# Kernel tuning notes

Measured on AMD Instinct MI355X. Metric: run time of the kernel, lower is better.

## Reference

```python
import jax, jax.numpy as jnp
import numpy as np

NHEAD, HEAD_DIM, UNFOLD = 16, 64, 3
SCALE = np.float32(1.0 / np.sqrt(HEAD_DIM))


def setup_inputs() -> dict:
    key = jax.random.key(0)
    ks = jax.random.split(key, 10)
    B, C, N, L, aL = 1, 256, 64, 256, 2
    D = NHEAD * HEAD_DIM  # 1024
    return {
        "x": jax.random.normal(ks[0], (B, C, N, L, 1), dtype=jnp.float32),
        "ax": jax.random.normal(ks[1], (B, C, N, aL, L), dtype=jnp.float32),
        "wq": jax.random.normal(ks[2], (D, C), dtype=jnp.float32) * 0.02,
        "bq": jax.random.normal(ks[3], (D,), dtype=jnp.float32) * 0.02,
        "wk": jax.random.normal(ks[4], (D, C), dtype=jnp.float32) * 0.02,
        "bk": jax.random.normal(ks[5], (D,), dtype=jnp.float32) * 0.02,
        "wv": jax.random.normal(ks[6], (D, C), dtype=jnp.float32) * 0.02,
        "bv": jax.random.normal(ks[7], (D,), dtype=jnp.float32) * 0.02,
        "wo": jax.random.normal(ks[8], (C, D), dtype=jnp.float32) * 0.02,
        "bo": jax.random.normal(ks[9], (C,), dtype=jnp.float32) * 0.02,
    }


def _proj(x, w, b):
    # x: [B,C,N,L], w: [D,C] -> [B,D,N,L]  (1x1x1 Conv3d == pointwise GEMM)
    return jnp.einsum('bcnl,dc->bdnl', x, w) + b[None, :, None, None]


def reference(x, ax, wq, bq, wk, bk, wv, bv, wo, bo):
    B, C, N, L, _ = x.shape
    x4 = x[..., 0]  # [B,C,N,L]
    q = _proj(x4, wq, bq).reshape(B, NHEAD, HEAD_DIM, N, 1, L)
    k4 = _proj(x4, wk, bk)
    v4 = _proj(x4, wv, bv)

    def unfold(t):
        # F.unfold kernel (3,1), padding (1,0) along N, then the original's
        # .view(B, nhead, head_dim, N, 3, L) applied to [B, C*3, N*L]
        tp = jnp.pad(t, ((0, 0), (0, 0), (1, 1), (0, 0)))
        tw = jnp.stack([tp[:, :, i:i + N, :] for i in range(UNFOLD)], axis=2)  # [B,D,3,N,L]
        return tw.reshape(B, NHEAD, HEAD_DIM, UNFOLD, N, L).reshape(
            B, NHEAD, HEAD_DIM, N, UNFOLD, L)

    k = unfold(k4)
    v = unfold(v4)

    aL = ax.shape[3]
    ak = (jnp.einsum('bcnal,dc->bdnal', ax, wk)
          + bk[None, :, None, None, None]).reshape(B, NHEAD, HEAD_DIM, N, aL, L)
    av = (jnp.einsum('bcnal,dc->bdnal', ax, wv)
          + bv[None, :, None, None, None]).reshape(B, NHEAD, HEAD_DIM, N, aL, L)
    k = jnp.concatenate([k, ak], axis=4)  # [B,H,d,N,3+aL,L]
    v = jnp.concatenate([v, av], axis=4)

    scores = (q * k).sum(2, keepdims=True) * SCALE        # [B,H,1,N,W,L]
    alphas = jax.nn.softmax(scores, axis=4)               # dropout=eval -> identity
    att = (alphas * v).sum(4).reshape(B, NHEAD * HEAD_DIM, N, L)
    out = jnp.einsum('bdnl,cd->bcnl', att, wo) + bo[None, :, None, None]
    return out[..., None]  # [B,nhid,N,L,1]
```

## Files before the change

kernel.cpp:

```cpp
#include <hip/hip_runtime.h>
#include <hip/hip_bf16.h>
#include <stdint.h>

#define N_HEAD 16
#define HDIM 64
#define C_IN 256
#define D_MODEL 1024
#define N_SP 64
#define L_SP 256
#define A_L 2
#define MS (N_SP * L_SP)
#define MA (N_SP * A_L * L_SP)
#define MT (MS + MA)
#define ATT_SCALE 0.125f
#define AUXP 136
#define CTP 136

typedef __attribute__((ext_vector_type(8))) short bf16x8;
typedef __attribute__((ext_vector_type(4))) float f32x4;
typedef __attribute__((ext_vector_type(8))) unsigned short u16x8;
typedef __attribute__((ext_vector_type(4))) unsigned int u32x4;

static __device__ __forceinline__ __hip_bfloat16 f2bf(float v) { return __float2bfloat16(v); }
static __device__ __forceinline__ unsigned short bfbits(float v) {
    union { __hip_bfloat16 h; unsigned short u; } cv;
    cv.h = __float2bfloat16(v);
    return cv.u;
}
static __device__ __forceinline__ float s2f(short u) {
    union { unsigned int i; float f; } c;
    c.i = ((unsigned int)(unsigned short)u) << 16;
    return c.f;
}

__global__ __launch_bounds__(256) void prep_weights(
    const float* __restrict__ wq, const float* __restrict__ bq,
    const float* __restrict__ wk, const float* __restrict__ bk,
    const float* __restrict__ wv, const float* __restrict__ bv,
    const float* __restrict__ wo,
    __hip_bfloat16* __restrict__ Wqkv, float* __restrict__ BiasQKV,
    __hip_bfloat16* __restrict__ WoB)
{
    int idx = blockIdx.x * 256 + threadIdx.x;
    int row = idx >> 8, col = idx & 255;
    const float* w = (row < D_MODEL) ? wq : (row < 2 * D_MODEL) ? wk : wv;
    Wqkv[idx] = f2bf(w[(size_t)(row & (D_MODEL - 1)) * C_IN + col]);
    if (col == 0) {
        const float* b = (row < D_MODEL) ? bq : (row < 2 * D_MODEL) ? bk : bv;
        BiasQKV[row] = b[row & (D_MODEL - 1)];
    }
    if (idx < C_IN * D_MODEL) WoB[idx] = f2bf(wo[idx]);
}

__global__ __launch_bounds__(256) void transpose_in(
    const float* __restrict__ x, const float* __restrict__ ax,
    __hip_bfloat16* __restrict__ XtAll)
{
    __shared__ float tile[32][33];
    const int tx = threadIdx.x, ty = threadIdx.y;
    const int bx = blockIdx.x;
    const float* src; int M, m0, drow0;
    if (bx < MS / 32) { src = x;  M = MS; m0 = bx * 32;              drow0 = m0; }
    else              { src = ax; M = MA; m0 = (bx - MS / 32) * 32;  drow0 = MS + m0; }
    const int c0 = blockIdx.y * 32;
#pragma unroll
    for (int j = 0; j < 32; j += 8)
        tile[ty + j][tx] = src[(size_t)(c0 + ty + j) * M + m0 + tx];
    __syncthreads();
#pragma unroll
    for (int j = 0; j < 32; j += 8)
        XtAll[(size_t)(drow0 + ty + j) * C_IN + c0 + tx] = f2bf(tile[tx][ty + j]);
}

__global__ __launch_bounds__(256) void gemm_proj(
    const __hip_bfloat16* __restrict__ A,
    const __hip_bfloat16* __restrict__ B,
    __hip_bfloat16* __restrict__ C,
    const float* __restrict__ bias,
    int M, int N, int K)
{
    __shared__ __align__(16) char lds[128 * CTP * 2];
    __hip_bfloat16* As = (__hip_bfloat16*)lds;
    __hip_bfloat16* Bs = As + 128 * 64;
    __hip_bfloat16* Ct = (__hip_bfloat16*)lds;

    const int tid = threadIdx.x;
    const int lane = tid & 63;
    const int w = tid >> 6;
    const int wr = w >> 1, wc = w & 1;
    const int fr = lane & 15, fq = lane >> 4;

    const int nwg = gridDim.x * gridDim.y;
    const int lin = blockIdx.y * gridDim.x + blockIdx.x;
    const int qq = nwg >> 3, rr = nwg & 7;
    const int xcd = lin & 7, ix = lin >> 3;
    const int nlin = (xcd < rr) ? xcd * (qq + 1) + ix
                                : rr * (qq + 1) + (xcd - rr) * qq + ix;
    const int bx = nlin % gridDim.x, by = nlin / gridDim.x;

    const int i0 = by * 128, j0 = bx * 128;
    const int srow = tid >> 3, sch = (tid & 7) << 3;
    const int scolsw = sch ^ ((srow & 7) << 3);
    const int rdsw = (fr & 7) << 3;

    f32x4 acc[4][4];
#pragma unroll
    for (int a = 0; a < 4; ++a)
#pragma unroll
        for (int b = 0; b < 4; ++b) acc[a][b] = (f32x4){0.f, 0.f, 0.f, 0.f};

    for (int k0 = 0; k0 < K; k0 += 64) {
        u32x4 ra[4], rb[4];
#pragma unroll
        for (int is = 0; is < 4; ++is) {
            int row = is * 32 + srow;
            ra[is] = *(const u32x4*)(A + (size_t)(i0 + row) * K + k0 + sch);
            rb[is] = *(const u32x4*)(B + (size_t)(j0 + row) * K + k0 + sch);
        }
#pragma unroll
        for (int is = 0; is < 4; ++is) {
            int row = is * 32 + srow;
            *(u32x4*)(As + row * 64 + scolsw) = ra[is];
            *(u32x4*)(Bs + row * 64 + scolsw) = rb[is];
        }
        __syncthreads();
#pragma unroll
        for (int kk = 0; kk < 64; kk += 32) {
            bf16x8 af[4], bb[4];
#pragma unroll
            for (int mi = 0; mi < 4; ++mi)
                af[mi] = *(const bf16x8*)(As + (wr * 64 + mi * 16 + fr) * 64 + ((kk + fq * 8) ^ rdsw));
#pragma unroll
            for (int ni = 0; ni < 4; ++ni)
                bb[ni] = *(const bf16x8*)(Bs + (wc * 64 + ni * 16 + fr) * 64 + ((kk + fq * 8) ^ rdsw));
#pragma unroll
            for (int mi = 0; mi < 4; ++mi)
#pragma unroll
                for (int ni = 0; ni < 4; ++ni)
                    acc[mi][ni] = __builtin_amdgcn_mfma_f32_16x16x32_bf16(
                        af[mi], bb[ni], acc[mi][ni], 0, 0, 0);
        }
        __syncthreads();
    }

    float bcol[4];
#pragma unroll
    for (int ni = 0; ni < 4; ++ni) bcol[ni] = bias[j0 + wc * 64 + ni * 16 + fr];
#pragma unroll
    for (int mi = 0; mi < 4; ++mi)
#pragma unroll
        for (int r = 0; r < 4; ++r) {
            int row = wr * 64 + mi * 16 + fq * 4 + r;
#pragma unroll
            for (int ni = 0; ni < 4; ++ni)
                Ct[row * CTP + wc * 64 + ni * 16 + fr] = f2bf(acc[mi][ni][r] + bcol[ni]);
        }
    __syncthreads();

    const int rr2 = tid >> 4, cc2 = (tid & 15) << 3;
#pragma unroll
    for (int pass = 0; pass < 8; ++pass) {
        int row = pass * 16 + rr2;
        *(u16x8*)(C + (size_t)(i0 + row) * N + j0 + cc2) =
            *(const u16x8*)(Ct + row * CTP + cc2);
    }
}

__global__ __launch_bounds__(256) void attn_fused(
    const __hip_bfloat16* __restrict__ XtAll,
    const __hip_bfloat16* __restrict__ Wqkv,
    const float* __restrict__ BiasQKV,
    __hip_bfloat16* qkv)
{
    __shared__ __align__(16) char ldsraw[36864];
    __hip_bfloat16* As  = (__hip_bfloat16*)ldsraw;
    __hip_bfloat16* Bs  = (__hip_bfloat16*)(ldsraw + 16384);
    __hip_bfloat16* aux = (__hip_bfloat16*)ldsraw;

    const int flat = blockIdx.x;
    const int xcd = flat & 7, idx = flat >> 3;
    const int n  = xcd * 8 + (idx & 7);
    const int h  = (idx >> 3) & 15;
    const int lt = idx >> 7;

    const int tid = threadIdx.x;
    const int lane = tid & 63;
    const int w = tid >> 6;
    const int wr = w >> 1, wc = w & 1;
    const int fr = lane & 15, fq = lane >> 4;
    const int srow = tid >> 3, sch = (tid & 7) << 3;
    const int scolsw = sch ^ ((srow & 7) << 3);
    const int rdsw = (fr & 7) << 3;

    const int sub = tid & 3;
    const int ll = tid >> 2;
    const int l = lt * 64 + ll;
    const int m = n * L_SP + l;
    const int ch = sub * 16;

    int src[3]; float val[3];
#pragma unroll
    for (int wd = 0; wd < 3; ++wd) {
        int f = n * 3 + wd;
        int un = f >> 6;
        int nn = (f & 63) + un - 1;
        bool ok = (nn >= 0) && (nn < N_SP);
        src[wd] = ok ? nn : 0;
        val[wd] = ok ? 1.f : 0.f;
    }

    __hip_bfloat16* qp = qkv + (size_t)m * 3072 + h * 64 + ch;
    bf16x8 q0 = *(const bf16x8*)qp, q1 = *(const bf16x8*)(qp + 8);
    bf16x8 kg[3][2], vg[3][2];
#pragma unroll
    for (int wd = 0; wd < 3; ++wd) {
        const __hip_bfloat16* rowp = qkv + (size_t)(src[wd] * L_SP + l) * 3072 + h * 64 + ch;
        kg[wd][0] = *(const bf16x8*)(rowp + 1024);
        kg[wd][1] = *(const bf16x8*)(rowp + 1024 + 8);
        vg[wd][0] = *(const bf16x8*)(rowp + 2048);
        vg[wd][1] = *(const bf16x8*)(rowp + 2048 + 8);
    }

    f32x4 acc[4][4];
#pragma unroll
    for (int a = 0; a < 4; ++a)
#pragma unroll
        for (int b = 0; b < 4; ++b) acc[a][b] = (f32x4){0.f, 0.f, 0.f, 0.f};

    for (int k0 = 0; k0 < 256; k0 += 64) {
        u32x4 ra[4], rb[4];
#pragma unroll
        for (int is = 0; is < 4; ++is) {
            int r = is * 32 + srow;
            int arow = MS + n * 512 + (r >> 6) * 256 + lt * 64 + (r & 63);
            int brow = 1024 + (r >> 6) * 1024 + h * 64 + (r & 63);
            ra[is] = *(const u32x4*)(XtAll + (size_t)arow * 256 + k0 + sch);
            rb[is] = *(const u32x4*)(Wqkv + (size_t)brow * 256 + k0 + sch);
        }
#pragma unroll
        for (int is = 0; is < 4; ++is) {
            int r = is * 32 + srow;
            *(u32x4*)(As + r * 64 + scolsw) = ra[is];
            *(u32x4*)(Bs + r * 64 + scolsw) = rb[is];
        }
        __syncthreads();
#pragma unroll
        for (int kk = 0; kk < 64; kk += 32) {
            bf16x8 af[4], bb[4];
#pragma unroll
            for (int mi = 0; mi < 4; ++mi)
                af[mi] = *(const bf16x8*)(As + (wr * 64 + mi * 16 + fr) * 64 + ((kk + fq * 8) ^ rdsw));
#pragma unroll
            for (int ni = 0; ni < 4; ++ni)
                bb[ni] = *(const bf16x8*)(Bs + (wc * 64 + ni * 16 + fr) * 64 + ((kk + fq * 8) ^ rdsw));
#pragma unroll
            for (int mi = 0; mi < 4; ++mi)
#pragma unroll
                for (int ni = 0; ni < 4; ++ni)
                    acc[mi][ni] = __builtin_amdgcn_mfma_f32_16x16x32_bf16(
                        af[mi], bb[ni], acc[mi][ni], 0, 0, 0);
        }
        __syncthreads();
    }

    float bcol[4];
#pragma unroll
    for (int ni = 0; ni < 4; ++ni)
        bcol[ni] = BiasQKV[1024 + wc * 1024 + h * 64 + ni * 16 + fr];

#pragma unroll
    for (int mi = 0; mi < 4; ++mi)
#pragma unroll
        for (int r = 0; r < 4; ++r) {
            int row = wr * 64 + mi * 16 + fq * 4 + r;
#pragma unroll
            for (int ni = 0; ni < 4; ++ni) {
                int col = wc * 64 + ni * 16 + fr;
                aux[row * AUXP + col] = f2bf(acc[mi][ni][r] + bcol[ni]);
            }
        }
    __syncthreads();

    bf16x8 ka[2][2], va[2][2];
#pragma unroll
    for (int a = 0; a < 2; ++a) {
        const __hip_bfloat16* base = aux + (a * 64 + ll) * AUXP;
        ka[a][0] = *(const bf16x8*)(base + ch);
        ka[a][1] = *(const bf16x8*)(base + ch + 8);
        va[a][0] = *(const bf16x8*)(base + 64 + ch);
        va[a][1] = *(const bf16x8*)(base + 64 + ch + 8);
    }

    float s[5];
#pragma unroll
    for (int i = 0; i < 3; ++i) {
        float d = 0.f;
#pragma unroll
        for (int j = 0; j < 8; ++j)
            d += s2f(q0[j]) * s2f(kg[i][0][j]) + s2f(q1[j]) * s2f(kg[i][1][j]);
        s[i] = d;
    }
#pragma unroll
    for (int a = 0; a < 2; ++a) {
        float d = 0.f;
#pragma unroll
        for (int j = 0; j < 8; ++j)
            d += s2f(q0[j]) * s2f(ka[a][0][j]) + s2f(q1[j]) * s2f(ka[a][1][j]);
        s[3 + a] = d;
    }
#pragma unroll
    for (int i = 0; i < 5; ++i) {
        s[i] += __shfl_xor(s[i], 1);
        s[i] += __shfl_xor(s[i], 2);
        s[i] *= ATT_SCALE;
    }
    s[0] *= val[0]; s[1] *= val[1]; s[2] *= val[2];

    float mx = fmaxf(fmaxf(fmaxf(s[0], s[1]), fmaxf(s[2], s[3])), s[4]);
    float e0 = __expf(s[0] - mx), e1 = __expf(s[1] - mx), e2 = __expf(s[2] - mx);
    float e3 = __expf(s[3] - mx), e4 = __expf(s[4] - mx);
    float inv = 1.f / (e0 + e1 + e2 + e3 + e4);
    float al[5];
    al[0] = e0 * inv * val[0];
    al[1] = e1 * inv * val[1];
    al[2] = e2 * inv * val[2];
    al[3] = e3 * inv;
    al[4] = e4 * inv;

#pragma unroll
    for (int g = 0; g < 2; ++g) {
        u16x8 pack;
#pragma unroll
        for (int j = 0; j < 8; ++j) {
            float o = al[0] * s2f(vg[0][g][j]) + al[1] * s2f(vg[1][g][j])
                    + al[2] * s2f(vg[2][g][j]) + al[3] * s2f(va[0][g][j])
                    + al[4] * s2f(va[1][g][j]);
            pack[j] = bfbits(o);
        }
        *(u16x8*)(qp + g * 8) = pack;
    }
}

__global__ __launch_bounds__(256) void gemm_out(
    const __hip_bfloat16* __restrict__ A,
    const __hip_bfloat16* __restrict__ B,
    float* __restrict__ C,
    const float* __restrict__ bo)
{
    __shared__ __align__(16) __hip_bfloat16 As[128 * 64];
    __shared__ __align__(16) __hip_bfloat16 Bs[128 * 64];

    const int tid = threadIdx.x;
    const int lane = tid & 63;
    const int w = tid >> 6;
    const int wr = w >> 1, wc = w & 1;
    const int fr = lane & 15, fq = lane >> 4;

    const int nwg = gridDim.x * gridDim.y;
    const int lin = blockIdx.y * gridDim.x + blockIdx.x;
    const int qq = nwg >> 3, rr = nwg & 7;
    const int xcd = lin & 7, ix = lin >> 3;
    const int nlin = (xcd < rr) ? xcd * (qq + 1) + ix
                                : rr * (qq + 1) + (xcd - rr) * qq + ix;
    const int bx = nlin % gridDim.x, by = nlin / gridDim.x;

    const int i0 = by * 128, j0 = bx * 128;
    const int srow = tid >> 3, sch = (tid & 7) << 3;
    const int scolsw = sch ^ ((srow & 7) << 3);
    const int rdsw = (fr & 7) << 3;

    f32x4 acc[4][4];
#pragma unroll
    for (int a = 0; a < 4; ++a)
#pragma unroll
        for (int b = 0; b < 4; ++b) acc[a][b] = (f32x4){0.f, 0.f, 0.f, 0.f};

    for (int k0 = 0; k0 < 1024; k0 += 64) {
        u32x4 ra[4], rb[4];
#pragma unroll
        for (int is = 0; is < 4; ++is) {
            int row = is * 32 + srow;
            ra[is] = *(const u32x4*)(A + (size_t)(i0 + row) * 1024 + k0 + sch);
            rb[is] = *(const u32x4*)(B + (size_t)(j0 + row) * 3072 + k0 + sch);
        }
#pragma unroll
        for (int is = 0; is < 4; ++is) {
            int row = is * 32 + srow;
            *(u32x4*)(As + row * 64 + scolsw) = ra[is];
            *(u32x4*)(Bs + row * 64 + scolsw) = rb[is];
        }
        __syncthreads();
#pragma unroll
        for (int kk = 0; kk < 64; kk += 32) {
            bf16x8 af[4], bb[4];
#pragma unroll
            for (int mi = 0; mi < 4; ++mi)
                af[mi] = *(const bf16x8*)(As + (wr * 64 + mi * 16 + fr) * 64 + ((kk + fq * 8) ^ rdsw));
#pragma unroll
            for (int ni = 0; ni < 4; ++ni)
                bb[ni] = *(const bf16x8*)(Bs + (wc * 64 + ni * 16 + fr) * 64 + ((kk + fq * 8) ^ rdsw));
#pragma unroll
            for (int mi = 0; mi < 4; ++mi)
#pragma unroll
                for (int ni = 0; ni < 4; ++ni)
                    acc[mi][ni] = __builtin_amdgcn_mfma_f32_16x16x32_bf16(
                        af[mi], bb[ni], acc[mi][ni], 0, 0, 0);
        }
        __syncthreads();
    }

#pragma unroll
    for (int mi = 0; mi < 4; ++mi)
#pragma unroll
        for (int r = 0; r < 4; ++r) {
            int row = i0 + wr * 64 + mi * 16 + fq * 4 + r;
            float bv = bo[row];
#pragma unroll
            for (int ni = 0; ni < 4; ++ni) {
                int col = j0 + wc * 64 + ni * 16 + fr;
                C[(size_t)row * MS + col] = acc[mi][ni][r] + bv;
            }
        }
}

extern "C" void kernel_launch(void* const* d_in, const int* in_sizes, int n_in,
                              void* d_out, int out_size, void* d_ws, size_t ws_size,
                              hipStream_t stream) {
    const float* x  = (const float*)d_in[0];
    const float* ax = (const float*)d_in[1];
    const float* wq = (const float*)d_in[2];
    const float* bq = (const float*)d_in[3];
    const float* wk = (const float*)d_in[4];
    const float* bk = (const float*)d_in[5];
    const float* wv = (const float*)d_in[6];
    const float* bv = (const float*)d_in[7];
    const float* wo = (const float*)d_in[8];
    const float* bo = (const float*)d_in[9];

    auto pad = [](size_t b) { return (b + 255) & ~(size_t)255; };
    char* p = (char*)d_ws;
    auto alloc = [&](size_t bytes) { char* r = p; p += pad(bytes); return r; };

    __hip_bfloat16* Wqkv    = (__hip_bfloat16*)alloc((size_t)3 * D_MODEL * C_IN * 2);
    float*          BiasQKV = (float*)alloc((size_t)3 * D_MODEL * 4);
    __hip_bfloat16* WoB     = (__hip_bfloat16*)alloc((size_t)C_IN * D_MODEL * 2);
    __hip_bfloat16* XtAll   = (__hip_bfloat16*)alloc((size_t)MT * C_IN * 2);
    __hip_bfloat16* qkv_c   = (__hip_bfloat16*)alloc((size_t)MS * 3 * D_MODEL * 2);

    prep_weights<<<dim3(3 * D_MODEL * C_IN / 256), 256, 0, stream>>>(
        wq, bq, wk, bk, wv, bv, wo, Wqkv, BiasQKV, WoB);

    transpose_in<<<dim3(MT / 32, C_IN / 32), dim3(32, 8), 0, stream>>>(x, ax, XtAll);

    gemm_proj<<<dim3(3 * D_MODEL / 128, MS / 128), 256, 0, stream>>>(
        XtAll, Wqkv, qkv_c, BiasQKV, MS, 3 * D_MODEL, C_IN);

    attn_fused<<<dim3(N_SP * N_HEAD * 4), 256, 0, stream>>>(
        XtAll, Wqkv, BiasQKV, qkv_c);

    gemm_out<<<dim3(MS / 128, C_IN / 128), 256, 0, stream>>>(
        WoB, qkv_c, (float*)d_out, bo);
}
```

Measured before the change: 159.7 us.

## Load aux GEMM operands directly from global and stage output stores through LDS

In attn_fused, the auxiliary K/V projection GEMM now reads MFMA fragments straight from global memory into registers over a fully unrolled K loop. This removes the LDS staging tiles and their barriers, at the cost of uncoalesced, redundant global reads that rely on the cache. The GEMM also now runs before the neighbour K/V gathers. In gemm_out, the fp32 epilogue writes each half of the tile into a padded LDS buffer and then stores it to global as coalesced 16-byte vectors, replacing scattered 4-byte stores, at the cost of extra barriers.

```diff
diff --git a/kernel.cpp b/kernel.cpp
--- a/kernel.cpp
+++ b/kernel.cpp
@@ -15,6 +15,7 @@
 #define ATT_SCALE 0.125f
 #define AUXP 136
 #define CTP 136
+#define CTPF 132
 
 typedef __attribute__((ext_vector_type(8))) short bf16x8;
 typedef __attribute__((ext_vector_type(4))) float f32x4;
@@ -172,10 +173,7 @@
     const float* __restrict__ BiasQKV,
     __hip_bfloat16* qkv)
 {
-    __shared__ __align__(16) char ldsraw[36864];
-    __hip_bfloat16* As  = (__hip_bfloat16*)ldsraw;
-    __hip_bfloat16* Bs  = (__hip_bfloat16*)(ldsraw + 16384);
-    __hip_bfloat16* aux = (__hip_bfloat16*)ldsraw;
+    __shared__ __align__(16) __hip_bfloat16 aux[128 * AUXP];
 
     const int flat = blockIdx.x;
     const int xcd = flat & 7, idx = flat >> 3;
@@ -188,9 +186,60 @@
     const int w = tid >> 6;
     const int wr = w >> 1, wc = w & 1;
     const int fr = lane & 15, fq = lane >> 4;
-    const int srow = tid >> 3, sch = (tid & 7) << 3;
-    const int scolsw = sch ^ ((srow & 7) << 3);
-    const int rdsw = (fr & 7) << 3;
+
+    const __hip_bfloat16* arow[4];
+    const __hip_bfloat16* brow[4];
+#pragma unroll
+    for (int mi = 0; mi < 4; ++mi) {
+        int r = wr * 64 + mi * 16 + fr;
+        int ar = MS + n * 512 + (r >> 6) * 256 + lt * 64 + (r & 63);
+        arow[mi] = XtAll + (size_t)ar * 256 + fq * 8;
+    }
+#pragma unroll
+    for (int ni = 0; ni < 4; ++ni) {
+        int c = wc * 64 + ni * 16 + fr;
+        int br = 1024 + (c >> 6) * 1024 + h * 64 + (c & 63);
+        brow[ni] = Wqkv + (size_t)br * 256 + fq * 8;
+    }
+
+    f32x4 acc[4][4];
+#pragma unroll
+    for (int a = 0; a < 4; ++a)
+#pragma unroll
+        for (int b = 0; b < 4; ++b) acc[a][b] = (f32x4){0.f, 0.f, 0.f, 0.f};
+
+#pragma unroll
+    for (int k0 = 0; k0 < 256; k0 += 32) {
+        bf16x8 af[4], bb[4];
+#pragma unroll
+        for (int mi = 0; mi < 4; ++mi) af[mi] = *(const bf16x8*)(arow[mi] + k0);
+#pragma unroll
+        for (int ni = 0; ni < 4; ++ni) bb[ni] = *(const bf16x8*)(brow[ni] + k0);
+#pragma unroll
+        for (int mi = 0; mi < 4; ++mi)
+#pragma unroll
+            for (int ni = 0; ni < 4; ++ni)
+                acc[mi][ni] = __builtin_amdgcn_mfma_f32_16x16x32_bf16(
+                    af[mi], bb[ni], acc[mi][ni], 0, 0, 0);
+    }
+
+    float bcol[4];
+#pragma unroll
+    for (int ni = 0; ni < 4; ++ni)
+        bcol[ni] = BiasQKV[1024 + wc * 1024 + h * 64 + ni * 16 + fr];
+
+#pragma unroll
+    for (int mi = 0; mi < 4; ++mi)
+#pragma unroll
+        for (int r = 0; r < 4; ++r) {
+            int row = wr * 64 + mi * 16 + fq * 4 + r;
+#pragma unroll
+            for (int ni = 0; ni < 4; ++ni) {
+                int col = wc * 64 + ni * 16 + fr;
+                aux[row * AUXP + col] = f2bf(acc[mi][ni][r] + bcol[ni]);
+            }
+        }
+    __syncthreads();
 
     const int sub = tid & 3;
     const int ll = tid >> 2;
@@ -211,6 +260,7 @@
 
     __hip_bfloat16* qp = qkv + (size_t)m * 3072 + h * 64 + ch;
     bf16x8 q0 = *(const bf16x8*)qp, q1 = *(const bf16x8*)(qp + 8);
+
     bf16x8 kg[3][2], vg[3][2];
 #pragma unroll
     for (int wd = 0; wd < 3; ++wd) {
@@ -220,67 +270,6 @@
         vg[wd][0] = *(const bf16x8*)(rowp + 2048);
         vg[wd][1] = *(const bf16x8*)(rowp + 2048 + 8);
     }
-
-    f32x4 acc[4][4];
-#pragma unroll
-    for (int a = 0; a < 4; ++a)
-#pragma unroll
-        for (int b = 0; b < 4; ++b) acc[a][b] = (f32x4){0.f, 0.f, 0.f, 0.f};
-
-    for (int k0 = 0; k0 < 256; k0 += 64) {
-        u32x4 ra[4], rb[4];
-#pragma unroll
-        for (int is = 0; is < 4; ++is) {
-            int r = is * 32 + srow;
-            int arow = MS + n * 512 + (r >> 6) * 256 + lt * 64 + (r & 63);
-            int brow = 1024 + (r >> 6) * 1024 + h * 64 + (r & 63);
-            ra[is] = *(const u32x4*)(XtAll + (size_t)arow * 256 + k0 + sch);
-            rb[is] = *(const u32x4*)(Wqkv + (size_t)brow * 256 + k0 + sch);
-        }
-#pragma unroll
-        for (int is = 0; is < 4; ++is) {
-            int r = is * 32 + srow;
-            *(u32x4*)(As + r * 64 + scolsw) = ra[is];
-            *(u32x4*)(Bs + r * 64 + scolsw) = rb[is];
-        }
-        __syncthreads();
-#pragma unroll
-        for (int kk = 0; kk < 64; kk += 32) {
-            bf16x8 af[4], bb[4];
-#pragma unroll
-            for (int mi = 0; mi < 4; ++mi)
-                af[mi] = *(const bf16x8*)(As + (wr * 64 + mi * 16 + fr) * 64 + ((kk + fq * 8) ^ rdsw));
-#pragma unroll
-            for (int ni = 0; ni < 4; ++ni)
-                bb[ni] = *(const bf16x8*)(Bs + (wc * 64 + ni * 16 + fr) * 64 + ((kk + fq * 8) ^ rdsw));
-#pragma unroll
-            for (int mi = 0; mi < 4; ++mi)
-#pragma unroll
-                for (int ni = 0; ni < 4; ++ni)
-                    acc[mi][ni] = __builtin_amdgcn_mfma_f32_16x16x32_bf16(
-                        af[mi], bb[ni], acc[mi][ni], 0, 0, 0);
-        }
-        __syncthreads();
-    }
-
-    float bcol[4];
-#pragma unroll
-    for (int ni = 0; ni < 4; ++ni)
-        bcol[ni] = BiasQKV[1024 + wc * 1024 + h * 64 + ni * 16 + fr];
-
-#pragma unroll
-    for (int mi = 0; mi < 4; ++mi)
-#pragma unroll
-        for (int r = 0; r < 4; ++r) {
-            int row = wr * 64 + mi * 16 + fq * 4 + r;
-#pragma unroll
-            for (int ni = 0; ni < 4; ++ni) {
-                int col = wc * 64 + ni * 16 + fr;
-                aux[row * AUXP + col] = f2bf(acc[mi][ni][r] + bcol[ni]);
-            }
-        }
-    __syncthreads();
-
     bf16x8 ka[2][2], va[2][2];
 #pragma unroll
     for (int a = 0; a < 2; ++a) {
@@ -347,8 +336,10 @@
     float* __restrict__ C,
     const float* __restrict__ bo)
 {
-    __shared__ __align__(16) __hip_bfloat16 As[128 * 64];
-    __shared__ __align__(16) __hip_bfloat16 Bs[128 * 64];
+    __shared__ __align__(16) char lds[64 * CTPF * 4];
+    __hip_bfloat16* As = (__hip_bfloat16*)lds;
+    __hip_bfloat16* Bs = As + 128 * 64;
+    float* Ctf = (float*)lds;
 
     const int tid = threadIdx.x;
     const int lane = tid & 63;
@@ -410,17 +401,29 @@
     }
 
 #pragma unroll
-    for (int mi = 0; mi < 4; ++mi)
-#pragma unroll
-        for (int r = 0; r < 4; ++r) {
-            int row = i0 + wr * 64 + mi * 16 + fq * 4 + r;
-            float bv = bo[row];
-#pragma unroll
-            for (int ni = 0; ni < 4; ++ni) {
-                int col = j0 + wc * 64 + ni * 16 + fr;
-                C[(size_t)row * MS + col] = acc[mi][ni][r] + bv;
-            }
-        }
+    for (int half = 0; half < 2; ++half) {
+        if (wr == half) {
+#pragma unroll
+            for (int mi = 0; mi < 4; ++mi)
+#pragma unroll
+                for (int r = 0; r < 4; ++r) {
+                    int lrow = mi * 16 + fq * 4 + r;
+                    float bv = bo[i0 + half * 64 + lrow];
+#pragma unroll
+                    for (int ni = 0; ni < 4; ++ni)
+                        Ctf[lrow * CTPF + wc * 64 + ni * 16 + fr] = acc[mi][ni][r] + bv;
+                }
+        }
+        __syncthreads();
+#pragma unroll
+        for (int it = 0; it < 8; ++it) {
+            int lrow = it * 8 + (tid >> 5);
+            int g = tid & 31;
+            *(f32x4*)(C + (size_t)(i0 + half * 64 + lrow) * MS + j0 + g * 4) =
+                *(const f32x4*)(Ctf + lrow * CTPF + g * 4);
+        }
+        __syncthreads();
+    }
 }
 
 extern "C" void kernel_launch(void* const* d_in, const int* in_sizes, int n_in,
```

After: 218.3 us. +36.7%, slower.
